# Optimization experiments

Hardware: AMD Instinct MI355X
Metric: run time of the kernel (lower is better)

The kernel has to match this reference:

```python
import jax, jax.numpy as jnp
import numpy as np

D_MODEL = 1024
N_HEADS = 16
D_KEYS = 64
GROUP_POSITIONS = [list(range(g * 32, (g + 1) * 32)) for g in range(4)]


def _make_tables(group_positions, dim):
    # InGroup table: pe[j,i] = (j/Lg) * L0 / 10000^(2*(i//2)/dim)
    L0 = len(group_positions[0])
    rows = []
    for grp in group_positions:
        Lg = len(grp)
        for j in range(Lg):
            rows.append([j / Lg * L0 / np.power(10000.0, 2 * (i // 2) / dim) for i in range(dim)])
    pe = np.array(rows)
    ingroup = np.concatenate([np.sin(pe[:, 0::2]), np.cos(pe[:, 1::2])], axis=1).astype(np.float32)
    # Sequence (group) table: pe[j,i] = grp[0] / 10000^(j/Lg), constant over i
    rows = []
    for grp in group_positions:
        Lg = len(grp)
        for j in range(Lg):
            rows.append([grp[0] / np.power(10000.0, j / Lg) for _ in range(dim)])
    pe = np.array(rows)
    seq = np.concatenate([np.sin(pe[:, 0::2]), np.cos(pe[:, 1::2])], axis=1).astype(np.float32)
    return jnp.asarray(ingroup), jnp.asarray(seq)


def setup_inputs() -> dict:
    key = jax.random.key(0)
    ks = jax.random.split(key, 12)
    B, L, S = 64, 128, 128
    dqk = D_KEYS * N_HEADS
    sc_in = 1.0 / np.sqrt(D_MODEL)
    sc_out = 1.0 / np.sqrt(dqk)
    inp = {
        "queries": jax.random.normal(ks[0], (B, L, D_MODEL), jnp.float32),
        "keys": jax.random.normal(ks[1], (B, S, D_MODEL), jnp.float32),
        "values": jax.random.normal(ks[2], (B, S, D_MODEL), jnp.float32),
        "attn_mask": jnp.zeros((B, 1, L, S), dtype=bool),
        "Wq": jax.random.normal(ks[3], (D_MODEL, dqk), jnp.float32) * sc_in,
        "bq": jnp.zeros((dqk,), jnp.float32),
        "Wk": jax.random.normal(ks[4], (D_MODEL, dqk), jnp.float32) * sc_in,
        "bk": jnp.zeros((dqk,), jnp.float32),
        "Wv": jax.random.normal(ks[5], (D_MODEL, dqk), jnp.float32) * sc_in,
        "bv": jnp.zeros((dqk,), jnp.float32),
        "Wo": jax.random.normal(ks[6], (dqk, D_MODEL), jnp.float32) * sc_out,
        "bo": jnp.zeros((D_MODEL,), jnp.float32),
    }
    pos_ingroup, pos_seq = _make_tables(GROUP_POSITIONS, D_KEYS)
    inp["pos_ingroup"] = pos_ingroup  # [n_pos, d_keys]
    inp["pos_seq"] = pos_seq          # [n_pos, d_keys]
    return inp


def _rope(x, pos):
    # x: [B, H, L, D]; pos: [L, D]
    sin, cos = jnp.split(pos, 2, axis=-1)
    sin_pos = jnp.stack([sin, sin], axis=-1).reshape(pos.shape)
    cos_pos = jnp.stack([cos, cos], axis=-1).reshape(pos.shape)
    rot = jnp.stack([-x[..., 1::2], x[..., ::2]], axis=-1).reshape(x.shape)
    return x * cos_pos + rot * sin_pos


def reference(queries, keys, values, attn_mask, Wq, bq, Wk, bk, Wv, bv, Wo, bo, pos_ingroup, pos_seq):
    B, L, _ = queries.shape
    S = keys.shape[1]
    H, E = N_HEADS, D_KEYS
    q = (queries @ Wq + bq).reshape(B, L, H, E).transpose(0, 2, 1, 3)  # [B,H,L,E]
    k = (keys @ Wk + bk).reshape(B, S, H, E).transpose(0, 2, 1, 3)
    v = (values @ Wv + bv).reshape(B, S, H, E).transpose(0, 2, 1, 3)
    # group-sequence in-group RoPE, then group RoPE (tables gathered at arange positions)
    q = _rope(_rope(q, pos_ingroup[:L]), pos_seq[:L])
    k = _rope(_rope(k, pos_ingroup[:S]), pos_seq[:S])
    # inner full attention on [B,L,H,E] layout
    scale = 1.0 / jnp.sqrt(jnp.asarray(E, q.dtype))
    scores = jnp.einsum("bhle,bhse->bhls", q, k) * scale
    scores = jnp.where(attn_mask, jnp.asarray(-jnp.inf, scores.dtype), scores)
    attn = jax.nn.softmax(scores, axis=-1)  # [B,H,L,S]
    out = jnp.einsum("bhls,bhsd->blhd", attn, v).reshape(B, L, H * E)
    return out @ Wo + bo, attn
```

## Files before the change

kernel.cpp:

```cpp
#include <hip/hip_runtime.h>
#include <cstdint>

typedef float f32x4 __attribute__((ext_vector_type(4)));
typedef __bf16 bf16x8 __attribute__((ext_vector_type(8)));
typedef unsigned short u16x8 __attribute__((ext_vector_type(8)));

typedef __attribute__((address_space(3))) uint32_t lds_u32;
typedef __attribute__((address_space(1))) const uint32_t glb_u32;

#define GLOAD_LDS16(gp, lp) \
  __builtin_amdgcn_global_load_lds((glb_u32*)(uintptr_t)(gp), (lds_u32*)(uintptr_t)(lp), 16, 0, 0)

__device__ inline unsigned short f2bf(float f) {
  union { float f; uint32_t u; } v; v.f = f;
  uint32_t u = v.u;
  return (unsigned short)((u + 0x7fffu + ((u >> 16) & 1u)) >> 16);
}

__global__ void prep_w(const float* __restrict__ wq, const float* __restrict__ wk,
                       const float* __restrict__ wv, const float* __restrict__ wo,
                       unsigned short* __restrict__ wt)
{
  __shared__ float t[64][65];
  const int z = blockIdx.z;
  const float* W = (z == 0) ? wq : (z == 1) ? wk : (z == 2) ? wv : wo;
  unsigned short* Wt = wt + (size_t)z * 1048576;
  const int n0 = blockIdx.x * 64, k0 = blockIdx.y * 64;
  const int tx = threadIdx.x & 63, ty = threadIdx.x >> 6;
#pragma unroll
  for (int i = 0; i < 16; i++) {
    int row = i * 4 + ty;
    t[row][tx] = W[(size_t)(k0 + row) * 1024 + n0 + tx];
  }
  __syncthreads();
#pragma unroll
  for (int i = 0; i < 16; i++) {
    int row = i * 4 + ty;
    Wt[(size_t)(n0 + row) * 1024 + k0 + tx] = f2bf(t[tx][row]);
  }
}

__global__ void comb_kernel(const float* __restrict__ ing, const float* __restrict__ seq,
                            float* __restrict__ cosc, float* __restrict__ sinc)
{
  int idx = blockIdx.x * 256 + threadIdx.x;
  int j = idx >> 5, i = idx & 31;
  float s1 = ing[j * 64 + i], c1 = ing[j * 64 + 32 + i];
  float s2 = seq[j * 64 + i], c2 = seq[j * 64 + 32 + i];
  cosc[idx] = c1 * c2 - s1 * s2;
  sinc[idx] = s1 * c2 + c1 * s2;
}

__global__ __launch_bounds__(256, 2)
void gemm_qkv(const float* __restrict__ qf, const float* __restrict__ kf,
              const float* __restrict__ vf,
              const unsigned short* __restrict__ Bbase,
              const float* __restrict__ b0, const float* __restrict__ b1,
              const float* __restrict__ b2,
              unsigned short* __restrict__ qb, unsigned short* __restrict__ kb,
              unsigned short* __restrict__ vtb,
              const float* __restrict__ cosc, const float* __restrict__ sinc)
{
  __shared__ __attribute__((aligned(16))) float Asf[8192];
  __shared__ __attribute__((aligned(16))) unsigned short Bs[8192];

  const int tid = threadIdx.x;
  const int lane = tid & 63;
  const int wave = tid >> 6;
  const int quad = lane >> 4;
  const int l15 = lane & 15;

  const int z = blockIdx.z;
  const int tileM = blockIdx.x * 128;
  const int tileN = blockIdx.y * 128;
  const int K = 1024;

  const float* A = (z == 0) ? qf : (z == 1) ? kf : vf;
  const unsigned short* B = Bbase + (size_t)z * (1024u * 1024u);

  const int wm = (wave >> 1) * 64;
  const int wn = (wave & 1) * 64;

  f32x4 acc[4][4];
#pragma unroll
  for (int a = 0; a < 4; a++)
#pragma unroll
    for (int n = 0; n < 4; n++)
      acc[a][n] = (f32x4){0.f, 0.f, 0.f, 0.f};

  for (int k0 = 0; k0 < K; k0 += 64) {
#pragma unroll
    for (int cc = 0; cc < 8; cc++) {
      int c = wave * 8 + cc;
      int g = c * 64 + lane;
      int row = g >> 4;
      int gc = (g & 15) ^ (row & 15);
      const float* ga = A + (size_t)(tileM + row) * 1024 + k0 + gc * 4;
      GLOAD_LDS16(ga, &Asf[c * 256]);
    }
#pragma unroll
    for (int cc = 0; cc < 4; cc++) {
      int c = wave * 4 + cc;
      int s = c * 64 + lane;
      int row = s >> 3;
      int gc = (s & 7) ^ (row & 7);
      const unsigned short* gb = B + (size_t)(tileN + row) * K + k0 + gc * 8;
      GLOAD_LDS16(gb, &Bs[c * 512]);
    }
    __syncthreads();

#pragma unroll
    for (int ks = 0; ks < 2; ks++) {
      bf16x8 af[4], bfr[4];
#pragma unroll
      for (int a = 0; a < 4; a++) {
        int r = wm + a * 16 + l15;
        int L0 = ks * 8 + quad * 2;
        f32x4 fa = *(const f32x4*)&Asf[(r * 16 + (L0 ^ l15)) * 4];
        f32x4 fb = *(const f32x4*)&Asf[(r * 16 + ((L0 + 1) ^ l15)) * 4];
        af[a] = (bf16x8){(__bf16)fa[0], (__bf16)fa[1], (__bf16)fa[2], (__bf16)fa[3],
                         (__bf16)fb[0], (__bf16)fb[1], (__bf16)fb[2], (__bf16)fb[3]};
      }
#pragma unroll
      for (int n = 0; n < 4; n++) {
        int r = wn + n * 16 + l15;
        int cp = (ks * 4 + quad) ^ (r & 7);
        bfr[n] = *(const bf16x8*)&Bs[(r * 8 + cp) * 8];
      }
#pragma unroll
      for (int a = 0; a < 4; a++)
#pragma unroll
        for (int n = 0; n < 4; n++)
          acc[a][n] = __builtin_amdgcn_mfma_f32_16x16x32_bf16(af[a], bfr[n], acc[a][n], 0, 0, 0);
    }
    __syncthreads();
  }

  const float* bias = (z == 0) ? b0 : (z == 1) ? b1 : b2;
  unsigned short* outq = (z == 0) ? qb : kb;
  unsigned short* flat = (unsigned short*)Asf;

#pragma unroll
  for (int n = 0; n < 4; n++) {
    int lcg = wn + n * 16 + l15;
    float bv_ = bias[tileN + lcg];
    int e = lcg & 63;
#pragma unroll
    for (int a = 0; a < 4; a++)
#pragma unroll
      for (int reg = 0; reg < 4; reg++) {
        int l = wm + a * 16 + quad * 4 + reg;
        float v = acc[a][n][reg] + bv_;
        unsigned short ov;
        int f;
        if (z == 2) {
          ov = f2bf(v);
          f = lcg * 128 + l;
          f ^= ((f >> 7) & 15) << 3;
        } else {
          float other = __shfl_xor(v, 1);
          float cs = cosc[l * 32 + (e >> 1)];
          float sn = sinc[l * 32 + (e >> 1)];
          ov = f2bf(v * cs + ((e & 1) ? other : -other) * sn);
          f = ((lcg >> 6) << 13) + (l << 6) + e;
          f ^= ((f >> 8) & 7) << 4;
        }
        flat[f] = ov;
      }
  }
  __syncthreads();

  unsigned short* gout = ((z == 2) ? vtb : outq) +
                         ((size_t)(tileM >> 7) * 16 + (tileN >> 6)) * 8192;
#pragma unroll
  for (int c = 0; c < 8; c++) {
    int f0 = tid * 64 + c * 8;
    int s0 = (z == 2) ? (f0 ^ (((f0 >> 7) & 15) << 3))
                      : (f0 ^ (((f0 >> 8) & 7) << 4));
    *(u16x8*)&gout[f0] = *(const u16x8*)&flat[s0];
  }
}

__global__ __launch_bounds__(256, 2)
void gemm_bt(const unsigned short* __restrict__ Abase,
             const unsigned short* __restrict__ Bbase,
             const float* __restrict__ b0, const float* __restrict__ b1,
             const float* __restrict__ b2,
             unsigned short* __restrict__ qb, unsigned short* __restrict__ kb,
             unsigned short* __restrict__ vtb,
             float* __restrict__ outf,
             const float* __restrict__ cosc, const float* __restrict__ sinc,
             int final_mode)
{
  __shared__ __attribute__((aligned(16))) unsigned short Sh[2][8192];
  unsigned short* As = &Sh[0][0];
  unsigned short* Bs = &Sh[1][0];

  const int tid = threadIdx.x;
  const int lane = tid & 63;
  const int wave = tid >> 6;
  const int quad = lane >> 4;
  const int l15 = lane & 15;

  const int z = blockIdx.z;
  const int tileM = blockIdx.x * 128;
  const int tileN = blockIdx.y * 128;
  const int K = 1024;

  const unsigned short* A = Abase + (size_t)z * (8192u * 1024u);
  const unsigned short* B = Bbase + (size_t)z * (1024u * 1024u);

  const int wm = (wave >> 1) * 64;
  const int wn = (wave & 1) * 64;

  f32x4 acc[4][4];
#pragma unroll
  for (int a = 0; a < 4; a++)
#pragma unroll
    for (int n = 0; n < 4; n++)
      acc[a][n] = (f32x4){0.f, 0.f, 0.f, 0.f};

  for (int k0 = 0; k0 < K; k0 += 64) {
#pragma unroll
    for (int cc = 0; cc < 4; cc++) {
      int c = wave * 4 + cc;
      int s = c * 64 + lane;
      int row = s >> 3;
      int gc = (s & 7) ^ (row & 7);
      const unsigned short* ga = A + (size_t)(tileM + row) * K + k0 + gc * 8;
      const unsigned short* gb = B + (size_t)(tileN + row) * K + k0 + gc * 8;
      GLOAD_LDS16(ga, &As[c * 512]);
      GLOAD_LDS16(gb, &Bs[c * 512]);
    }
    __syncthreads();

#pragma unroll
    for (int ks = 0; ks < 2; ks++) {
      bf16x8 af[4], bfr[4];
#pragma unroll
      for (int a = 0; a < 4; a++) {
        int r = wm + a * 16 + l15;
        int cp = (ks * 4 + quad) ^ (r & 7);
        af[a] = *(const bf16x8*)&As[(r * 8 + cp) * 8];
      }
#pragma unroll
      for (int n = 0; n < 4; n++) {
        int r = wn + n * 16 + l15;
        int cp = (ks * 4 + quad) ^ (r & 7);
        bfr[n] = *(const bf16x8*)&Bs[(r * 8 + cp) * 8];
      }
#pragma unroll
      for (int a = 0; a < 4; a++)
#pragma unroll
        for (int n = 0; n < 4; n++)
          acc[a][n] = __builtin_amdgcn_mfma_f32_16x16x32_bf16(af[a], bfr[n], acc[a][n], 0, 0, 0);
    }
    __syncthreads();
  }

  if (final_mode) {
#pragma unroll
    for (int n = 0; n < 4; n++) {
      int cg = tileN + wn + n * 16 + l15;
      float bias = b0[cg];
#pragma unroll
      for (int a = 0; a < 4; a++)
#pragma unroll
        for (int reg = 0; reg < 4; reg++) {
          int r = tileM + wm + a * 16 + quad * 4 + reg;
          outf[(size_t)r * 1024 + cg] = acc[a][n][reg] + bias;
        }
    }
  } else {
    const float* bias = (z == 0) ? b0 : (z == 1) ? b1 : b2;
    unsigned short* outq = (z == 0) ? qb : kb;
    unsigned short* flat = &Sh[0][0];

#pragma unroll
    for (int n = 0; n < 4; n++) {
      int lcg = wn + n * 16 + l15;
      float bv_ = bias[tileN + lcg];
      int e = lcg & 63;
#pragma unroll
      for (int a = 0; a < 4; a++)
#pragma unroll
        for (int reg = 0; reg < 4; reg++) {
          int l = wm + a * 16 + quad * 4 + reg;
          float v = acc[a][n][reg] + bv_;
          unsigned short ov;
          int f;
          if (z == 2) {
            ov = f2bf(v);
            f = lcg * 128 + l;
            f ^= ((f >> 7) & 15) << 3;
          } else {
            float other = __shfl_xor(v, 1);
            float cs = cosc[l * 32 + (e >> 1)];
            float sn = sinc[l * 32 + (e >> 1)];
            ov = f2bf(v * cs + ((e & 1) ? other : -other) * sn);
            f = ((lcg >> 6) << 13) + (l << 6) + e;
            f ^= ((f >> 8) & 7) << 3;
          }
          flat[f] = ov;
        }
    }
    __syncthreads();

    unsigned short* gout = ((z == 2) ? vtb : outq) +
                           ((size_t)(tileM >> 7) * 16 + (tileN >> 6)) * 8192;
#pragma unroll
    for (int c = 0; c < 8; c++) {
      int f0 = tid * 64 + c * 8;
      int s0 = (z == 2) ? (f0 ^ (((f0 >> 7) & 15) << 3))
                        : (f0 ^ (((f0 >> 8) & 7) << 3));
      *(u16x8*)&gout[f0] = *(const u16x8*)&flat[s0];
    }
  }
}

__global__ __launch_bounds__(256, 2)
void attn_kernel(const unsigned short* __restrict__ qb,
                 const unsigned short* __restrict__ kb,
                 const unsigned short* __restrict__ vtb,
                 const unsigned char* __restrict__ mask,
                 float* __restrict__ attn_out,
                 unsigned short* __restrict__ ob)
{
  __shared__ __attribute__((aligned(16))) unsigned short Pb[128 * 136];
  const int tid = threadIdx.x;
  const int lane = tid & 63;
  const int wave = tid >> 6;
  const int quad = lane >> 4;
  const int l15 = lane & 15;
  const int bh = blockIdx.x;
  const int b = bh >> 4;
  const int h = bh & 15;

  const unsigned short* q = qb + (size_t)bh * 128 * 64;
  const unsigned short* k = kb + (size_t)bh * 128 * 64;
  const unsigned short* vt = vtb + (size_t)bh * 64 * 128;

  f32x4 sacc[2][8];
#pragma unroll
  for (int mt = 0; mt < 2; mt++)
#pragma unroll
    for (int nt = 0; nt < 8; nt++)
      sacc[mt][nt] = (f32x4){0.f, 0.f, 0.f, 0.f};

#pragma unroll
  for (int ks = 0; ks < 2; ks++) {
    bf16x8 aq[2], bk[8];
#pragma unroll
    for (int mt = 0; mt < 2; mt++)
      aq[mt] = *(const bf16x8*)&q[(size_t)(wave * 32 + mt * 16 + l15) * 64 + ks * 32 + quad * 8];
#pragma unroll
    for (int nt = 0; nt < 8; nt++)
      bk[nt] = *(const bf16x8*)&k[(size_t)(nt * 16 + l15) * 64 + ks * 32 + quad * 8];
#pragma unroll
    for (int mt = 0; mt < 2; mt++)
#pragma unroll
      for (int nt = 0; nt < 8; nt++)
        sacc[mt][nt] = __builtin_amdgcn_mfma_f32_16x16x32_bf16(aq[mt], bk[nt], sacc[mt][nt], 0, 0, 0);
  }

  const float scale = 0.125f;
#pragma unroll
  for (int mt = 0; mt < 2; mt++) {
#pragma unroll
    for (int reg = 0; reg < 4; reg++) {
      int r = wave * 32 + mt * 16 + quad * 4 + reg;
      const unsigned char* mrow = mask + ((size_t)b * 128 + r) * 128;
      float sv[8];
#pragma unroll
      for (int nt = 0; nt < 8; nt++) {
        float x = sacc[mt][nt][reg] * scale;
        if (mrow[nt * 16 + l15]) x = -__builtin_inff();
        sv[nt] = x;
      }
      float m = sv[0];
#pragma unroll
      for (int nt = 1; nt < 8; nt++) m = fmaxf(m, sv[nt]);
#pragma unroll
      for (int off = 1; off < 16; off <<= 1) m = fmaxf(m, __shfl_xor(m, off));
      float s = 0.f;
#pragma unroll
      for (int nt = 0; nt < 8; nt++) { sv[nt] = __expf(sv[nt] - m); s += sv[nt]; }
#pragma unroll
      for (int off = 1; off < 16; off <<= 1) s += __shfl_xor(s, off);
      float inv = 1.0f / s;
      float* arow = attn_out + ((size_t)bh * 128 + r) * 128;
#pragma unroll
      for (int nt = 0; nt < 8; nt++) {
        float p = sv[nt] * inv;
        arow[nt * 16 + l15] = p;
        Pb[r * 136 + nt * 16 + l15] = f2bf(p);
      }
    }
  }
  __syncthreads();

  f32x4 oacc[2][4];
#pragma unroll
  for (int mt = 0; mt < 2; mt++)
#pragma unroll
    for (int nt = 0; nt < 4; nt++)
      oacc[mt][nt] = (f32x4){0.f, 0.f, 0.f, 0.f};

#pragma unroll
  for (int ks = 0; ks < 4; ks++) {
    bf16x8 bv[4], ap[2];
#pragma unroll
    for (int nt = 0; nt < 4; nt++)
      bv[nt] = *(const bf16x8*)&vt[(size_t)(nt * 16 + l15) * 128 + ks * 32 + quad * 8];
#pragma unroll
    for (int mt = 0; mt < 2; mt++)
      ap[mt] = *(const bf16x8*)&Pb[(size_t)(wave * 32 + mt * 16 + l15) * 136 + ks * 32 + quad * 8];
#pragma unroll
    for (int mt = 0; mt < 2; mt++)
#pragma unroll
      for (int nt = 0; nt < 4; nt++)
        oacc[mt][nt] = __builtin_amdgcn_mfma_f32_16x16x32_bf16(ap[mt], bv[nt], oacc[mt][nt], 0, 0, 0);
  }

#pragma unroll
  for (int mt = 0; mt < 2; mt++)
#pragma unroll
    for (int nt = 0; nt < 4; nt++)
#pragma unroll
      for (int reg = 0; reg < 4; reg++) {
        int r = wave * 32 + mt * 16 + quad * 4 + reg;
        int e = nt * 16 + l15;
        ob[((size_t)b * 128 + r) * 1024 + h * 64 + e] = f2bf(oacc[mt][nt][reg]);
      }
}

extern "C" void kernel_launch(void* const* d_in, const int* in_sizes, int n_in,
                              void* d_out, int out_size, void* d_ws, size_t ws_size,
                              hipStream_t stream)
{
  const float* queries = (const float*)d_in[0];
  const float* keys    = (const float*)d_in[1];
  const float* values  = (const float*)d_in[2];
  const unsigned char* mask = (const unsigned char*)d_in[3];
  const float* Wq = (const float*)d_in[4];
  const float* bq = (const float*)d_in[5];
  const float* Wk = (const float*)d_in[6];
  const float* bk = (const float*)d_in[7];
  const float* Wv = (const float*)d_in[8];
  const float* bv = (const float*)d_in[9];
  const float* Wo = (const float*)d_in[10];
  const float* bo = (const float*)d_in[11];
  const float* ping = (const float*)d_in[12];
  const float* pseq = (const float*)d_in[13];

  float* out  = (float*)d_out;
  float* attn = out + 8388608;

  char* ws = (char*)d_ws;
  unsigned short* Wt  = (unsigned short*)(ws);
  float* cosc = (float*)(ws + 8388608);
  float* sinc = (float*)(ws + 8388608 + 16384);
  unsigned short* qbuf = (unsigned short*)(ws + 8421376);
  unsigned short* kbuf = (unsigned short*)(ws + 8421376 + 16777216);
  unsigned short* vtbuf= (unsigned short*)(ws + 8421376 + 2*16777216);
  unsigned short* obuf = (unsigned short*)(ws + 8421376 + 3*16777216);

  prep_w<<<dim3(16, 16, 4), 256, 0, stream>>>(Wq, Wk, Wv, Wo, Wt);
  comb_kernel<<<16, 256, 0, stream>>>(ping, pseq, cosc, sinc);
  gemm_qkv<<<dim3(64, 8, 3), 256, 0, stream>>>(queries, keys, values, Wt,
                                               bq, bk, bv,
                                               qbuf, kbuf, vtbuf, cosc, sinc);
  attn_kernel<<<dim3(1024), 256, 0, stream>>>(qbuf, kbuf, vtbuf, mask, attn, obuf);
  gemm_bt<<<dim3(64, 8, 1), 256, 0, stream>>>(obuf, Wt + 3 * 1048576, bo, bo, bo,
                                              qbuf, kbuf, vtbuf, out,
                                              cosc, sinc, 1);
}
```

Baseline: 345.8 us.

## Pre-convert QKV inputs to bf16 and use 128x256 tiles in QKV GEMM

A new pass converts the fp32 query, key and value activations to bf16 in a scratch region that reuses the attention-output buffer. The QKV projection GEMM then loads bf16 A tiles directly and runs 512 threads over 128x256 tiles, writing its epilogue in two halves through shared memory. This removes the fp32 A staging and the per-fragment conversion inside the inner loop, and halves how often the A tiles are re-read. The cost is an extra full read and write pass over the activations, plus more shared memory and threads per block. The gemm_bt epilogue swizzle shift also changes from 3 to 4 to match the QKV kernel.

Result: no change. 344.3 us (-0.4%).

```diff
diff --git a/kernel.cpp b/kernel.cpp
--- a/kernel.cpp
+++ b/kernel.cpp
@@ -51,18 +51,31 @@
   sinc[idx] = s1 * c2 + c1 * s2;
 }
 
-__global__ __launch_bounds__(256, 2)
-void gemm_qkv(const float* __restrict__ qf, const float* __restrict__ kf,
-              const float* __restrict__ vf,
-              const unsigned short* __restrict__ Bbase,
-              const float* __restrict__ b0, const float* __restrict__ b1,
-              const float* __restrict__ b2,
-              unsigned short* __restrict__ qb, unsigned short* __restrict__ kb,
-              unsigned short* __restrict__ vtb,
-              const float* __restrict__ cosc, const float* __restrict__ sinc)
-{
-  __shared__ __attribute__((aligned(16))) float Asf[8192];
-  __shared__ __attribute__((aligned(16))) unsigned short Bs[8192];
+__global__ void cvt_kernel(const float* __restrict__ q, const float* __restrict__ k,
+                           const float* __restrict__ v, unsigned short* __restrict__ dst)
+{
+  const int z = blockIdx.z;
+  const float* src = (z == 0) ? q : (z == 1) ? k : v;
+  unsigned short* d = dst + (size_t)z * 8388608;
+  size_t i = ((size_t)blockIdx.x * 256 + threadIdx.x) * 4;
+  float4 f = *(const float4*)&src[i];
+  ushort4 o;
+  o.x = f2bf(f.x); o.y = f2bf(f.y); o.z = f2bf(f.z); o.w = f2bf(f.w);
+  *(ushort4*)&d[i] = o;
+}
+
+__global__ __launch_bounds__(512, 4)
+void gemm_qkv256(const unsigned short* __restrict__ Abase,
+                 const unsigned short* __restrict__ Bbase,
+                 const float* __restrict__ b0, const float* __restrict__ b1,
+                 const float* __restrict__ b2,
+                 unsigned short* __restrict__ qb, unsigned short* __restrict__ kb,
+                 unsigned short* __restrict__ vtb,
+                 const float* __restrict__ cosc, const float* __restrict__ sinc)
+{
+  __shared__ __attribute__((aligned(16))) unsigned short Sh[24576];
+  unsigned short* As = &Sh[0];
+  unsigned short* Bs = &Sh[8192];
 
   const int tid = threadIdx.x;
   const int lane = tid & 63;
@@ -72,14 +85,14 @@
 
   const int z = blockIdx.z;
   const int tileM = blockIdx.x * 128;
-  const int tileN = blockIdx.y * 128;
+  const int tileN = blockIdx.y * 256;
   const int K = 1024;
 
-  const float* A = (z == 0) ? qf : (z == 1) ? kf : vf;
+  const unsigned short* A = Abase + (size_t)z * (8192u * 1024u);
   const unsigned short* B = Bbase + (size_t)z * (1024u * 1024u);
 
-  const int wm = (wave >> 1) * 64;
-  const int wn = (wave & 1) * 64;
+  const int wm = (wave >> 2) * 64;
+  const int wn = (wave & 3) * 64;
 
   f32x4 acc[4][4];
 #pragma unroll
@@ -90,13 +103,12 @@
 
   for (int k0 = 0; k0 < K; k0 += 64) {
 #pragma unroll
-    for (int cc = 0; cc < 8; cc++) {
-      int c = wave * 8 + cc;
-      int g = c * 64 + lane;
-      int row = g >> 4;
-      int gc = (g & 15) ^ (row & 15);
-      const float* ga = A + (size_t)(tileM + row) * 1024 + k0 + gc * 4;
-      GLOAD_LDS16(ga, &Asf[c * 256]);
+    for (int cc = 0; cc < 2; cc++) {
+      int c = wave * 2 + cc;
+      int s = c * 64 + lane;
+      int row = s >> 3;
+      int gc = (s & 7) ^ (row & 7);
+      GLOAD_LDS16(A + (size_t)(tileM + row) * K + k0 + gc * 8, &As[c * 512]);
     }
 #pragma unroll
     for (int cc = 0; cc < 4; cc++) {
@@ -104,8 +116,7 @@
       int s = c * 64 + lane;
       int row = s >> 3;
       int gc = (s & 7) ^ (row & 7);
-      const unsigned short* gb = B + (size_t)(tileN + row) * K + k0 + gc * 8;
-      GLOAD_LDS16(gb, &Bs[c * 512]);
+      GLOAD_LDS16(B + (size_t)(tileN + row) * K + k0 + gc * 8, &Bs[c * 512]);
     }
     __syncthreads();
 
@@ -115,17 +126,14 @@
 #pragma unroll
       for (int a = 0; a < 4; a++) {
         int r = wm + a * 16 + l15;
-        int L0 = ks * 8 + quad * 2;
-        f32x4 fa = *(const f32x4*)&Asf[(r * 16 + (L0 ^ l15)) * 4];
-        f32x4 fb = *(const f32x4*)&Asf[(r * 16 + ((L0 + 1) ^ l15)) * 4];
-        af[a] = (bf16x8){(__bf16)fa[0], (__bf16)fa[1], (__bf16)fa[2], (__bf16)fa[3],
-                         (__bf16)fb[0], (__bf16)fb[1], (__bf16)fb[2], (__bf16)fb[3]};
+        int cp = (ks * 4 + quad) ^ (r & 7);
+        af[a] = *(const bf16x8*)&As[(r * 8 + cp) * 8];
       }
 #pragma unroll
       for (int n = 0; n < 4; n++) {
-        int r = wn + n * 16 + l15;
-        int cp = (ks * 4 + quad) ^ (r & 7);
-        bfr[n] = *(const bf16x8*)&Bs[(r * 8 + cp) * 8];
+        int rb = wn + n * 16 + l15;
+        int cp = (ks * 4 + quad) ^ (rb & 7);
+        bfr[n] = *(const bf16x8*)&Bs[(rb * 8 + cp) * 8];
       }
 #pragma unroll
       for (int a = 0; a < 4; a++)
@@ -138,46 +146,52 @@
 
   const float* bias = (z == 0) ? b0 : (z == 1) ? b1 : b2;
   unsigned short* outq = (z == 0) ? qb : kb;
-  unsigned short* flat = (unsigned short*)Asf;
-
-#pragma unroll
-  for (int n = 0; n < 4; n++) {
-    int lcg = wn + n * 16 + l15;
-    float bv_ = bias[tileN + lcg];
-    int e = lcg & 63;
-#pragma unroll
-    for (int a = 0; a < 4; a++)
-#pragma unroll
-      for (int reg = 0; reg < 4; reg++) {
-        int l = wm + a * 16 + quad * 4 + reg;
-        float v = acc[a][n][reg] + bv_;
-        unsigned short ov;
-        int f;
-        if (z == 2) {
-          ov = f2bf(v);
-          f = lcg * 128 + l;
-          f ^= ((f >> 7) & 15) << 3;
-        } else {
-          float other = __shfl_xor(v, 1);
-          float cs = cosc[l * 32 + (e >> 1)];
-          float sn = sinc[l * 32 + (e >> 1)];
-          ov = f2bf(v * cs + ((e & 1) ? other : -other) * sn);
-          f = ((lcg >> 6) << 13) + (l << 6) + e;
-          f ^= ((f >> 8) & 7) << 4;
-        }
-        flat[f] = ov;
-      }
-  }
-  __syncthreads();
-
-  unsigned short* gout = ((z == 2) ? vtb : outq) +
-                         ((size_t)(tileM >> 7) * 16 + (tileN >> 6)) * 8192;
-#pragma unroll
-  for (int c = 0; c < 8; c++) {
-    int f0 = tid * 64 + c * 8;
-    int s0 = (z == 2) ? (f0 ^ (((f0 >> 7) & 15) << 3))
-                      : (f0 ^ (((f0 >> 8) & 7) << 4));
-    *(u16x8*)&gout[f0] = *(const u16x8*)&flat[s0];
+  unsigned short* flat = &Sh[0];
+
+#pragma unroll
+  for (int p = 0; p < 2; p++) {
+    __syncthreads();
+    if (((wave >> 1) & 1) == p) {
+#pragma unroll
+      for (int n = 0; n < 4; n++) {
+        int lc = (wave & 1) * 64 + n * 16 + l15;
+        int cg = tileN + p * 128 + lc;
+        float bv_ = bias[cg];
+        int e = cg & 63;
+#pragma unroll
+        for (int a = 0; a < 4; a++)
+#pragma unroll
+          for (int reg = 0; reg < 4; reg++) {
+            int l = wm + a * 16 + quad * 4 + reg;
+            float v = acc[a][n][reg] + bv_;
+            unsigned short ov;
+            int f;
+            if (z == 2) {
+              ov = f2bf(v);
+              f = lc * 128 + l;
+              f ^= ((f >> 7) & 15) << 3;
+            } else {
+              float other = __shfl_xor(v, 1);
+              float cs = cosc[l * 32 + (e >> 1)];
+              float sn = sinc[l * 32 + (e >> 1)];
+              ov = f2bf(v * cs + ((e & 1) ? other : -other) * sn);
+              f = ((lc >> 6) << 13) + (l << 6) + e;
+              f ^= ((f >> 8) & 7) << 4;
+            }
+            flat[f] = ov;
+          }
+      }
+    }
+    __syncthreads();
+    unsigned short* gout = ((z == 2) ? vtb : outq) +
+        ((size_t)(tileM >> 7) * 16 + (tileN >> 6) + p * 2) * 8192;
+#pragma unroll
+    for (int c = 0; c < 4; c++) {
+      int f0 = (c * 512 + tid) * 8;
+      int s0 = (z == 2) ? (f0 ^ (((f0 >> 7) & 15) << 3))
+                        : (f0 ^ (((f0 >> 8) & 7) << 4));
+      *(u16x8*)&gout[f0] = *(const u16x8*)&flat[s0];
+    }
   }
 }
 
@@ -299,7 +313,7 @@
             float sn = sinc[l * 32 + (e >> 1)];
             ov = f2bf(v * cs + ((e & 1) ? other : -other) * sn);
             f = ((lcg >> 6) << 13) + (l << 6) + e;
-            f ^= ((f >> 8) & 7) << 3;
+            f ^= ((f >> 8) & 7) << 4;
           }
           flat[f] = ov;
         }
@@ -312,7 +326,7 @@
     for (int c = 0; c < 8; c++) {
       int f0 = tid * 64 + c * 8;
       int s0 = (z == 2) ? (f0 ^ (((f0 >> 7) & 15) << 3))
-                        : (f0 ^ (((f0 >> 8) & 7) << 3));
+                        : (f0 ^ (((f0 >> 8) & 7) << 4));
       *(u16x8*)&gout[f0] = *(const u16x8*)&flat[s0];
     }
   }
@@ -455,6 +469,7 @@
 
   float* out  = (float*)d_out;
   float* attn = out + 8388608;
+  unsigned short* Xbf = (unsigned short*)attn;
 
   char* ws = (char*)d_ws;
   unsigned short* Wt  = (unsigned short*)(ws);
@@ -467,9 +482,9 @@
 
   prep_w<<<dim3(16, 16, 4), 256, 0, stream>>>(Wq, Wk, Wv, Wo, Wt);
   comb_kernel<<<16, 256, 0, stream>>>(ping, pseq, cosc, sinc);
-  gemm_qkv<<<dim3(64, 8, 3), 256, 0, stream>>>(queries, keys, values, Wt,
-                                               bq, bk, bv,
-                                               qbuf, kbuf, vtbuf, cosc, sinc);
+  cvt_kernel<<<dim3(8192, 1, 3), 256, 0, stream>>>(queries, keys, values, Xbf);
+  gemm_qkv256<<<dim3(64, 4, 3), 512, 0, stream>>>(Xbf, Wt, bq, bk, bv,
+                                                  qbuf, kbuf, vtbuf, cosc, sinc);
   attn_kernel<<<dim3(1024), 256, 0, stream>>>(qbuf, kbuf, vtbuf, mask, attn, obuf);
   gemm_bt<<<dim3(64, 8, 1), 256, 0, stream>>>(obuf, Wt + 3 * 1048576, bo, bo, bo,
                                               qbuf, kbuf, vtbuf, out,
```
